# Performance work log

Measured on AMD Instinct MI355X. Metric: run time of the kernel, lower is better.

The kernel has to match this reference:

```python
import jax, jax.numpy as jnp
import numpy as np

C = 256          # channels
NUM_HEADS = 4
HEAD_DIM = C // NUM_HEADS
TILE_SIZE = 64
TILE_SEQ = TILE_SIZE * TILE_SIZE  # 4096
B, H_IMG, W_IMG = 1, 96, 96
EPS = 1e-5


def setup_inputs() -> dict:
    key = jax.random.key(0)
    k0, k1, k2 = jax.random.split(key, 3)
    x = jax.random.normal(k0, (B, C, H_IMG, W_IMG), jnp.float32)
    norm_w = jnp.ones((C,), jnp.float32)
    norm_b = jnp.zeros((C,), jnp.float32)
    qkv_w = jax.random.normal(k1, (3 * C, C), jnp.float32) * (C ** -0.5)
    qkv_b = jnp.zeros((3 * C,), jnp.float32)
    proj_w = jax.random.normal(k2, (C, C), jnp.float32) * (C ** -0.5)
    proj_b = jnp.zeros((C,), jnp.float32)
    return {"x": x, "norm_w": norm_w, "norm_b": norm_b,
            "qkv_w": qkv_w, "qkv_b": qkv_b,
            "proj_w": proj_w, "proj_b": proj_b}


def _attn(q, k, v, scale):
    # q: [B,H,Q,D], k/v: [B,H,K,D]
    s = jnp.einsum('bhqd,bhkd->bhqk', q, k) * scale
    p = jax.nn.softmax(s, axis=-1)
    return jnp.einsum('bhqk,bhkd->bhqd', p, v)


def reference(x, norm_w, norm_b, qkv_w, qkv_b, proj_w, proj_b):
    b, c, h, w = x.shape
    seq = h * w
    g = min(32, c)
    # GroupNorm
    xg = x.reshape(b, g, c // g, h, w)
    mean = xg.mean(axis=(2, 3, 4), keepdims=True)
    var = ((xg - mean) ** 2).mean(axis=(2, 3, 4), keepdims=True)
    xn = (xg - mean) * jax.lax.rsqrt(var + EPS)
    xn = xn.reshape(b, c, h, w) * norm_w[None, :, None, None] + norm_b[None, :, None, None]
    # flatten spatial -> tokens
    xf = xn.transpose(0, 2, 3, 1).reshape(b, seq, c)
    qkv = xf @ qkv_w.T + qkv_b  # [B,S,3C]
    qkv = qkv.reshape(b, seq, 3, NUM_HEADS, HEAD_DIM).transpose(2, 0, 3, 1, 4)
    q, k, v = qkv[0], qkv[1], qkv[2]  # [B,H,S,D]
    scale = HEAD_DIM ** -0.5
    if seq > TILE_SEQ:
        num_tiles = (seq + TILE_SEQ - 1) // TILE_SEQ
        outs = []
        for i in range(num_tiles):  # small fixed tile count, static slices
            s0 = i * TILE_SEQ
            e0 = min((i + 1) * TILE_SEQ, seq)
            k0 = max(0, s0 - TILE_SEQ // 2)
            k1 = min(seq, e0 + TILE_SEQ // 2)
            outs.append(_attn(q[:, :, s0:e0], k[:, :, k0:k1], v[:, :, k0:k1], scale))
        out = jnp.concatenate(outs, axis=2)
    else:
        out = _attn(q, k, v, scale)
    out = out.transpose(0, 2, 1, 3).reshape(b, seq, c)
    out = out @ proj_w.T + proj_b
    out = out.reshape(b, h, w, c).transpose(0, 3, 1, 2)
    return out + x
```

## Files before the change

### kernel.cpp

```cpp
#include <hip/hip_runtime.h>

typedef __bf16 bf16x8 __attribute__((ext_vector_type(8)));
typedef float f32x4 __attribute__((ext_vector_type(4)));
typedef float f32x16 __attribute__((ext_vector_type(16)));
typedef int i32x4 __attribute__((ext_vector_type(4)));
typedef int i32x2 __attribute__((ext_vector_type(2)));
typedef unsigned short u16x4 __attribute__((ext_vector_type(4)));

#define S_TOK 9216
#define LOG2E 1.44269504088896340736f
#define SCALE_Q (0.125f * LOG2E)

__device__ inline unsigned short f2bf(float f) {
    unsigned int u = __builtin_bit_cast(unsigned int, f);
    return (unsigned short)((u + 0x7fffu + ((u >> 16) & 1u)) >> 16);
}

__device__ inline unsigned int cvt_pk_bf16(float lo, float hi) {
    unsigned int r;
    asm("v_cvt_pk_bf16_f32 %0, %1, %2" : "=v"(r) : "v"(lo), "v"(hi));
    return r;
}

__device__ inline void permswap(unsigned int& a, unsigned int& b) {
    asm("v_permlane32_swap_b32 %0, %1" : "+v"(a), "+v"(b));
}

__device__ inline f32x4 MFMA(bf16x8 a, bf16x8 b, f32x4 c) {
    return __builtin_amdgcn_mfma_f32_16x16x32_bf16(a, b, c, 0, 0, 0);
}
__device__ inline f32x16 MFMA32(bf16x8 a, bf16x8 b, f32x16 c) {
    return __builtin_amdgcn_mfma_f32_32x32x16_bf16(a, b, c, 0, 0, 0);
}

__device__ inline int swz(int row, int c) {
    return ((c + (row >> 3)) & 7) ^ (row & 7);
}
__device__ inline bf16x8 load_frag(const unsigned short* lds, int outer, int kbase) {
    int lane = threadIdx.x & 63;
    int row = outer + (lane & 15);
    int cc = swz(row, (kbase >> 3) + (lane >> 4));
    return *reinterpret_cast<const bf16x8*>(lds + row * 64 + cc * 8);
}
__device__ inline bf16x8 load_frag32(const unsigned short* lds, int outer, int kbase) {
    int lane = threadIdx.x & 63;
    int row = outer + (lane & 31);
    int cc = swz(row, (kbase >> 3) + (lane >> 5));
    return *reinterpret_cast<const bf16x8*>(lds + row * 64 + cc * 8);
}
__device__ inline void stage_tile(unsigned short* lds, const unsigned short* src,
                                  int stride, int nrows) {
    for (int id = threadIdx.x; id < nrows * 8; id += 256) {
        int row = id >> 3, cc = id & 7;
        i32x4 v = *reinterpret_cast<const i32x4*>(src + row * stride + cc * 8);
        *reinterpret_cast<i32x4*>(lds + row * 64 + swz(row, cc) * 8) = v;
    }
}

__global__ __launch_bounds__(256) void gn_stats_part(const float* __restrict__ x,
                                                     float* __restrict__ part) {
    int c = blockIdx.x;
    const f32x4* p = reinterpret_cast<const f32x4*>(x + c * S_TOK);
    float s = 0.f, ss = 0.f;
    for (int i = threadIdx.x; i < 2304; i += 256) {
        f32x4 v = p[i];
        s += v[0] + v[1] + v[2] + v[3];
        ss += v[0] * v[0] + v[1] * v[1] + v[2] * v[2] + v[3] * v[3];
    }
#pragma unroll
    for (int off = 1; off < 64; off <<= 1) {
        s += __shfl_xor(s, off);
        ss += __shfl_xor(ss, off);
    }
    __shared__ float rs[4], rss[4];
    int wave = threadIdx.x >> 6;
    if ((threadIdx.x & 63) == 0) { rs[wave] = s; rss[wave] = ss; }
    __syncthreads();
    if (threadIdx.x == 0) {
        part[c] = rs[0] + rs[1] + rs[2] + rs[3];
        part[256 + c] = rss[0] + rss[1] + rss[2] + rss[3];
    }
}

__global__ __launch_bounds__(256) void gn_apply(const float* __restrict__ x,
                                                const float* __restrict__ part,
                                                const float* __restrict__ nw,
                                                const float* __restrict__ nb,
                                                unsigned short* __restrict__ xf) {
    __shared__ float tl[64][65];
    __shared__ float gmean[8], grstd[8];
    int sb = blockIdx.x * 64, cb = blockIdx.y * 64;
    if (threadIdx.x < 8) {
        int g = (cb >> 3) + threadIdx.x;
        float s = 0.f, ss = 0.f;
#pragma unroll
        for (int i = 0; i < 8; ++i) { s += part[g * 8 + i]; ss += part[256 + g * 8 + i]; }
        float mean = s * (1.f / 73728.f);
        float var = ss * (1.f / 73728.f) - mean * mean;
        gmean[threadIdx.x] = mean;
        grstd[threadIdx.x] = rsqrtf(var + 1e-5f);
    }
    __syncthreads();
    for (int id = threadIdx.x; id < 1024; id += 256) {
        int cr = id >> 4;
        int sq = (id & 15) << 2;
        int c = cb + cr;
        f32x4 v = *reinterpret_cast<const f32x4*>(x + c * S_TOK + sb + sq);
        float mu = gmean[cr >> 3], rstd = grstd[cr >> 3];
        float wv = nw[c] * rstd;
        float bv = nb[c] - mu * wv;
#pragma unroll
        for (int j = 0; j < 4; ++j) tl[sq + j][cr] = v[j] * wv + bv;
    }
    __syncthreads();
    for (int id = threadIdx.x; id < 1024; id += 256) {
        int sr = id >> 4;
        int cq = (id & 15) << 2;
        u16x4 o;
#pragma unroll
        for (int j = 0; j < 4; ++j) o[j] = f2bf(tl[sr][cq + j]);
        *reinterpret_cast<u16x4*>(xf + (sb + sr) * 256 + cb + cq) = o;
    }
}

__global__ __launch_bounds__(256) void conv_both(const float* __restrict__ qkvw_in,
                                                 const float* __restrict__ projw_in,
                                                 unsigned short* __restrict__ out) {
    int i = blockIdx.x * 256 + threadIdx.x;
    float v;
    if (i < 768 * 256) v = qkvw_in[i] * ((i < 256 * 256) ? SCALE_Q : 1.0f);
    else v = projw_in[i - 768 * 256];
    out[i] = f2bf(v);
}

template <int MODE>
__global__ __launch_bounds__(256) void gemm_bt(const unsigned short* __restrict__ A,
                                               const unsigned short* __restrict__ B,
                                               const float* __restrict__ bias,
                                               unsigned short* __restrict__ q_out,
                                               unsigned short* __restrict__ k_out,
                                               unsigned short* __restrict__ vT_out,
                                               const float* __restrict__ xres,
                                               float* __restrict__ out) {
    __shared__ alignas(16) unsigned short As[128 * 64];
    __shared__ alignas(16) unsigned short Bs[128 * 64];
    int mb = blockIdx.x, nb = blockIdx.y;
    int wave = threadIdx.x >> 6, lane = threadIdx.x & 63;
    int wm = wave >> 1, wn = wave & 1;
    f32x4 zero = {0.f, 0.f, 0.f, 0.f};
    f32x4 acc[4][4];
    for (int i = 0; i < 4; ++i)
        for (int j = 0; j < 4; ++j) acc[i][j] = zero;
    for (int ks = 0; ks < 4; ++ks) {
        __syncthreads();
        stage_tile(As, A + (mb * 128) * 256 + ks * 64, 256, 128);
        stage_tile(Bs, B + (nb * 128) * 256 + ks * 64, 256, 128);
        __syncthreads();
#pragma unroll
        for (int kk = 0; kk < 2; ++kk) {
            bf16x8 af[4], bfr[4];
#pragma unroll
            for (int mt = 0; mt < 4; ++mt) af[mt] = load_frag(As, wm * 64 + mt * 16, kk * 32);
#pragma unroll
            for (int nt = 0; nt < 4; ++nt) bfr[nt] = load_frag(Bs, wn * 64 + nt * 16, kk * 32);
#pragma unroll
            for (int mt = 0; mt < 4; ++mt)
#pragma unroll
                for (int nt = 0; nt < 4; ++nt)
                    acc[mt][nt] = MFMA(af[mt], bfr[nt], acc[mt][nt]);
        }
    }
    int r0 = (lane >> 4) << 2;
    int cl = lane & 15;
#pragma unroll
    for (int mt = 0; mt < 4; ++mt) {
#pragma unroll
        for (int nt = 0; nt < 4; ++nt) {
            int m = mb * 128 + wm * 64 + mt * 16 + r0;
            int n = nb * 128 + wn * 64 + nt * 16 + cl;
            if (MODE == 0) {
                float bv = bias[n] * ((n < 256) ? SCALE_Q : 1.0f);
                if (n < 256) {
#pragma unroll
                    for (int r = 0; r < 4; ++r)
                        q_out[(m + r) * 256 + n] = f2bf(acc[mt][nt][r] + bv);
                } else if (n < 512) {
#pragma unroll
                    for (int r = 0; r < 4; ++r)
                        k_out[(m + r) * 256 + (n - 256)] = f2bf(acc[mt][nt][r] + bv);
                } else {
                    u16x4 o;
#pragma unroll
                    for (int r = 0; r < 4; ++r) o[r] = f2bf(acc[mt][nt][r] + bv);
                    *reinterpret_cast<u16x4*>(vT_out + (n - 512) * S_TOK + m) = o;
                }
            } else {
                float bv = bias[n];
                f32x4 xr = *reinterpret_cast<const f32x4*>(xres + n * S_TOK + m);
                f32x4 o;
#pragma unroll
                for (int r = 0; r < 4; ++r) o[r] = acc[mt][nt][r] + bv + xr[r];
                *reinterpret_cast<f32x4*>(out + n * S_TOK + m) = o;
            }
        }
    }
}

struct StageRegs { i32x4 k0, k1, v0, v1; };

__device__ inline StageRegs load_stage(const unsigned short* ksrc, const unsigned short* vsrc) {
    int tid = threadIdx.x;
    int row = tid >> 3, cc = tid & 7;
    StageRegs r;
    r.k0 = *reinterpret_cast<const i32x4*>(ksrc + row * 256 + cc * 8);
    r.k1 = *reinterpret_cast<const i32x4*>(ksrc + (row + 32) * 256 + cc * 8);
    r.v0 = *reinterpret_cast<const i32x4*>(vsrc + row * S_TOK + cc * 8);
    r.v1 = *reinterpret_cast<const i32x4*>(vsrc + (row + 32) * S_TOK + cc * 8);
    return r;
}

__device__ inline void store_stage(unsigned short* K, unsigned short* V, StageRegs r) {
    int tid = threadIdx.x;
    int row = tid >> 3, cc = tid & 7;
    *reinterpret_cast<i32x4*>(K + row * 64 + swz(row, cc) * 8) = r.k0;
    *reinterpret_cast<i32x4*>(K + (row + 32) * 64 + swz(row + 32, cc) * 8) = r.k1;
    *reinterpret_cast<i32x4*>(V + row * 64 + swz(row, cc) * 8) = r.v0;
    *reinterpret_cast<i32x4*>(V + (row + 32) * 64 + swz(row + 32, cc) * 8) = r.v1;
}

template <int NC>
__global__ __launch_bounds__(256) void attn(const unsigned short* __restrict__ qb,
                                            const unsigned short* __restrict__ kb,
                                            const unsigned short* __restrict__ vT,
                                            unsigned short* __restrict__ Opart,
                                            float* __restrict__ lpart) {
    __shared__ alignas(16) unsigned short Ks[2][64 * 64];
    __shared__ alignas(16) unsigned short Vs[2][64 * 64];
    constexpr int NS0 = 96 / NC, NS1 = 112 / NC, NS2 = 48 / NC;
    constexpr int B0 = 32 * NS0, B1 = B0 + 32 * NS1, NB = B1 + 8 * NS2;
    static_assert(NC % 2 == 0 && NC >= 4, "NC even");

    int bx = blockIdx.x;
    int head = bx / NB;
    int r = bx % NB;
    int tile, seg, qi;
    if (r < B0)      { tile = 0; seg = r >> 5; qi = r & 31; }
    else if (r < B1) { int t = r - B0; tile = 1; seg = t >> 5; qi = t & 31; }
    else             { int t = r - B1; tile = 2; seg = t >> 3; qi = t & 7; }
    int qs0 = (tile == 0) ? 0 : (tile == 1 ? 4096 : 8192);
    int kv0 = (tile == 0) ? 0 : (tile == 1 ? 2048 : 6144);
    int qstart = qs0 + qi * 128;
    int c0 = seg * NC;
    int wave = threadIdx.x >> 6, lane = threadIdx.x & 63;
    int l31 = lane & 31, h = lane >> 5;

    stage_tile((unsigned short*)Ks, qb + qstart * 256 + head * 64, 256, 128);
    __syncthreads();
    bf16x8 qf[4];
#pragma unroll
    for (int s = 0; s < 4; ++s) qf[s] = load_frag32((unsigned short*)Ks, wave * 32, s * 16);
    __syncthreads();

    bf16x8 ones;
#pragma unroll
    for (int i = 0; i < 8; ++i) ones[i] = (__bf16)1.0f;

    f32x16 oacc0, oacc1, lac;
#pragma unroll
    for (int i = 0; i < 16; ++i) { oacc0[i] = 0.f; oacc1[i] = 0.f; lac[i] = 0.f; }

    const unsigned short* kbase = kb + kv0 * 256 + head * 64;
    const unsigned short* vbase = vT + head * 64 * S_TOK + kv0;

    auto compute = [&](const unsigned short* Kp, const unsigned short* Vp) {
        __builtin_amdgcn_s_setprio(1);
#pragma unroll
        for (int half = 0; half < 2; ++half) {
            f32x16 sc;
#pragma unroll
            for (int i = 0; i < 16; ++i) sc[i] = 0.f;
#pragma unroll
            for (int s = 0; s < 4; ++s)
                sc = MFMA32(load_frag32(Kp, half * 32, s * 16), qf[s], sc);
#pragma unroll
            for (int sl = 0; sl < 2; ++sl) {
                const int b = 8 * sl;
                float E[8];
#pragma unroll
                for (int i = 0; i < 8; ++i) E[i] = __builtin_amdgcn_exp2f(sc[b + i]);
                unsigned int w0 = cvt_pk_bf16(E[0], E[1]);
                unsigned int w1 = cvt_pk_bf16(E[2], E[3]);
                unsigned int w2 = cvt_pk_bf16(E[4], E[5]);
                unsigned int w3 = cvt_pk_bf16(E[6], E[7]);
                permswap(w0, w2);
                permswap(w1, w3);
                i32x4 w;
                w[0] = (int)w0; w[1] = (int)w1; w[2] = (int)w2; w[3] = (int)w3;
                bf16x8 pa = __builtin_bit_cast(bf16x8, w);
                int kvb = (half * 2 + sl) * 16;
                bf16x8 v0 = load_frag32(Vp, 0, kvb);
                bf16x8 v1 = load_frag32(Vp, 32, kvb);
                oacc0 = MFMA32(pa, v0, oacc0);
                oacc1 = MFMA32(pa, v1, oacc1);
                lac = MFMA32(pa, ones, lac);
            }
        }
        __builtin_amdgcn_s_setprio(0);
    };

    StageRegs Ra = load_stage(kbase + c0 * (64 * 256), vbase + c0 * 64);
    store_stage(Ks[0], Vs[0], Ra);
    Ra = load_stage(kbase + (c0 + 1) * (64 * 256), vbase + (c0 + 1) * 64);
    StageRegs Rb = load_stage(kbase + (c0 + 2 < c0 + NC ? c0 + 2 : c0) * (64 * 256),
                              vbase + (c0 + 2 < c0 + NC ? c0 + 2 : c0) * 64);
    __syncthreads();

#pragma unroll
    for (int k = 0; k < NC / 2; ++k) {
        int ch = c0 + 2 * k;
        store_stage(Ks[1], Vs[1], Ra);
        if (2 * k + 3 < NC)
            Ra = load_stage(kbase + (ch + 3) * (64 * 256), vbase + (ch + 3) * 64);
        compute(Ks[0], Vs[0]);
        __syncthreads();
        if (2 * k + 2 < NC) {
            store_stage(Ks[0], Vs[0], Rb);
            if (2 * k + 4 < NC)
                Rb = load_stage(kbase + (ch + 4) * (64 * 256), vbase + (ch + 4) * 64);
        }
        compute(Ks[1], Vs[1]);
        __syncthreads();
    }

    unsigned int obase = (unsigned int)seg * (S_TOK * 256);
#pragma unroll
    for (int reg = 0; reg < 16; ++reg) {
        int qloc = (reg & 3) + 8 * (reg >> 2) + 4 * h;
        int s = qstart + wave * 32 + qloc;
        Opart[obase + s * 256 + head * 64 + l31] =
            __builtin_bit_cast(unsigned short, (__bf16)oacc0[reg]);
        Opart[obase + s * 256 + head * 64 + 32 + l31] =
            __builtin_bit_cast(unsigned short, (__bf16)oacc1[reg]);
    }
    if (l31 == 0) {
#pragma unroll
        for (int reg = 0; reg < 16; ++reg) {
            int qloc = (reg & 3) + 8 * (reg >> 2) + 4 * h;
            int s = qstart + wave * 32 + qloc;
            lpart[(seg * 4 + head) * S_TOK + s] = lac[reg];
        }
    }
}

template <int NC>
__global__ __launch_bounds__(256) void combine(const unsigned short* __restrict__ Op,
                                               const float* __restrict__ lp,
                                               unsigned short* __restrict__ att) {
    int idx = blockIdx.x * 256 + threadIdx.x;
    int s = idx >> 5;
    int c0 = (idx & 31) << 3;
    int head = c0 >> 6;
    int nseg = (s < 4096) ? (96 / NC) : (s < 8192 ? (112 / NC) : (48 / NC));
    float acc[8] = {0.f, 0.f, 0.f, 0.f, 0.f, 0.f, 0.f, 0.f};
    float l = 0.f;
    for (int seg = 0; seg < nseg; ++seg) {
        i32x4 v = *reinterpret_cast<const i32x4*>(Op + (size_t)seg * (S_TOK * 256) + s * 256 + c0);
        const unsigned short* u = reinterpret_cast<const unsigned short*>(&v);
#pragma unroll
        for (int i = 0; i < 8; ++i)
            acc[i] += __builtin_bit_cast(float, ((unsigned int)u[i]) << 16);
        l += lp[(seg * 4 + head) * S_TOK + s];
    }
    float inv = 1.f / l;
    u16x4 o0, o1;
#pragma unroll
    for (int i = 0; i < 4; ++i) {
        o0[i] = f2bf(acc[i] * inv);
        o1[i] = f2bf(acc[4 + i] * inv);
    }
    unsigned short* dst = att + s * 256 + c0;
    *reinterpret_cast<u16x4*>(dst) = o0;
    *reinterpret_cast<u16x4*>(dst + 4) = o1;
}

extern "C" void kernel_launch(void* const* d_in, const int* in_sizes, int n_in,
                              void* d_out, int out_size, void* d_ws, size_t ws_size,
                              hipStream_t stream) {
    const float* x      = (const float*)d_in[0];
    const float* norm_w = (const float*)d_in[1];
    const float* norm_b = (const float*)d_in[2];
    const float* qkv_w  = (const float*)d_in[3];
    const float* qkv_b  = (const float*)d_in[4];
    const float* proj_w = (const float*)d_in[5];
    const float* proj_b = (const float*)d_in[6];
    float* outp = (float*)d_out;

    char* wsb = (char*)d_ws;
    float* part = (float*)wsb;
    unsigned short* xf    = (unsigned short*)(wsb + 2048);
    unsigned short* qkvw  = xf + 9216 * 256;
    unsigned short* projw = qkvw + 768 * 256;
    unsigned short* qbuf  = projw + 256 * 256;
    unsigned short* kbuf  = qbuf + 9216 * 256;
    unsigned short* vTbuf = kbuf + 9216 * 256;
    unsigned short* Opart = vTbuf + 256 * 9216;
    size_t fixed_bytes = 2048 + 2ull * 256 * (9216ull * 4 + 768 + 256);
    size_t need8 = fixed_bytes + 2ull * 14 * 9216 * 256 + 4ull * 14 * 4 * 9216;
    bool use8 = (ws_size >= need8);
    int MS = use8 ? 14 : 7;
    float* lpart = (float*)(Opart + (size_t)MS * 9216 * 256);
    unsigned short* attb  = xf;

    gn_stats_part<<<dim3(256), dim3(256), 0, stream>>>(x, part);
    gn_apply<<<dim3(144, 4), dim3(256), 0, stream>>>(x, part, norm_w, norm_b, xf);
    conv_both<<<dim3(1024), dim3(256), 0, stream>>>(qkv_w, proj_w, qkvw);
    gemm_bt<0><<<dim3(72, 6), dim3(256), 0, stream>>>(xf, qkvw, qkv_b,
                                                      qbuf, kbuf, vTbuf, nullptr, nullptr);
    if (use8) {
        attn<8><<<dim3(4 * 880), dim3(256), 0, stream>>>(qbuf, kbuf, vTbuf, Opart, lpart);
        combine<8><<<dim3(1152), dim3(256), 0, stream>>>(Opart, lpart, attb);
    } else {
        attn<16><<<dim3(4 * 440), dim3(256), 0, stream>>>(qbuf, kbuf, vTbuf, Opart, lpart);
        combine<16><<<dim3(1152), dim3(256), 0, stream>>>(Opart, lpart, attb);
    }
    gemm_bt<1><<<dim3(72, 2), dim3(256), 0, stream>>>(attb, projw, proj_b,
                                                      nullptr, nullptr, nullptr, x, outp);
}
```

Baseline: 149.4 us.

## Process two 32-row query tiles per wave to reuse K/V fragments

Each attention block now covers 256 query rows instead of 128, with every wave holding two Q fragment sets and two sets of output/denominator accumulators. Each K and V fragment read from LDS now feeds MFMAs for both query sub-tiles, halving K/V staging traffic per query row and halving the grid size. The double-buffered pipeline is simplified to a single-register prefetch per chunk. This raises register pressure, which may lower occupancy, and gives fewer blocks for load balancing.

```diff
diff --git a/kernel.cpp b/kernel.cpp
--- a/kernel.cpp
+++ b/kernel.cpp
@@ -228,46 +228,75 @@
     *reinterpret_cast<i32x4*>(V + (row + 32) * 64 + swz(row + 32, cc) * 8) = r.v1;
 }
 
+__device__ inline bf16x8 mkpa(const f32x16& sc, int b) {
+    float E0 = __builtin_amdgcn_exp2f(sc[b + 0]);
+    float E1 = __builtin_amdgcn_exp2f(sc[b + 1]);
+    float E2 = __builtin_amdgcn_exp2f(sc[b + 2]);
+    float E3 = __builtin_amdgcn_exp2f(sc[b + 3]);
+    float E4 = __builtin_amdgcn_exp2f(sc[b + 4]);
+    float E5 = __builtin_amdgcn_exp2f(sc[b + 5]);
+    float E6 = __builtin_amdgcn_exp2f(sc[b + 6]);
+    float E7 = __builtin_amdgcn_exp2f(sc[b + 7]);
+    unsigned int w0 = cvt_pk_bf16(E0, E1);
+    unsigned int w1 = cvt_pk_bf16(E2, E3);
+    unsigned int w2 = cvt_pk_bf16(E4, E5);
+    unsigned int w3 = cvt_pk_bf16(E6, E7);
+    permswap(w0, w2);
+    permswap(w1, w3);
+    i32x4 w;
+    w[0] = (int)w0; w[1] = (int)w1; w[2] = (int)w2; w[3] = (int)w3;
+    return __builtin_bit_cast(bf16x8, w);
+}
+
 template <int NC>
 __global__ __launch_bounds__(256) void attn(const unsigned short* __restrict__ qb,
                                             const unsigned short* __restrict__ kb,
                                             const unsigned short* __restrict__ vT,
                                             unsigned short* __restrict__ Opart,
                                             float* __restrict__ lpart) {
-    __shared__ alignas(16) unsigned short Ks[2][64 * 64];
-    __shared__ alignas(16) unsigned short Vs[2][64 * 64];
+    __shared__ alignas(16) unsigned short LDS[4 * 4096];
+    unsigned short* Ks0 = LDS;
+    unsigned short* Ks1 = LDS + 4096;
+    unsigned short* Vs0 = LDS + 8192;
+    unsigned short* Vs1 = LDS + 12288;
     constexpr int NS0 = 96 / NC, NS1 = 112 / NC, NS2 = 48 / NC;
-    constexpr int B0 = 32 * NS0, B1 = B0 + 32 * NS1, NB = B1 + 8 * NS2;
+    constexpr int B0 = 16 * NS0, B1 = B0 + 16 * NS1, NB = B1 + 4 * NS2;
     static_assert(NC % 2 == 0 && NC >= 4, "NC even");
 
     int bx = blockIdx.x;
     int head = bx / NB;
     int r = bx % NB;
     int tile, seg, qi;
-    if (r < B0)      { tile = 0; seg = r >> 5; qi = r & 31; }
-    else if (r < B1) { int t = r - B0; tile = 1; seg = t >> 5; qi = t & 31; }
-    else             { int t = r - B1; tile = 2; seg = t >> 3; qi = t & 7; }
+    if (r < B0)      { tile = 0; seg = r >> 4; qi = r & 15; }
+    else if (r < B1) { int t = r - B0; tile = 1; seg = t >> 4; qi = t & 15; }
+    else             { int t = r - B1; tile = 2; seg = t >> 2; qi = t & 3; }
     int qs0 = (tile == 0) ? 0 : (tile == 1 ? 4096 : 8192);
     int kv0 = (tile == 0) ? 0 : (tile == 1 ? 2048 : 6144);
-    int qstart = qs0 + qi * 128;
+    int qstart = qs0 + qi * 256;
     int c0 = seg * NC;
     int wave = threadIdx.x >> 6, lane = threadIdx.x & 63;
     int l31 = lane & 31, h = lane >> 5;
 
-    stage_tile((unsigned short*)Ks, qb + qstart * 256 + head * 64, 256, 128);
-    __syncthreads();
-    bf16x8 qf[4];
-#pragma unroll
-    for (int s = 0; s < 4; ++s) qf[s] = load_frag32((unsigned short*)Ks, wave * 32, s * 16);
+    stage_tile(LDS, qb + qstart * 256 + head * 64, 256, 256);
+    __syncthreads();
+    bf16x8 qfA[4], qfB[4];
+#pragma unroll
+    for (int s = 0; s < 4; ++s) {
+        qfA[s] = load_frag32(LDS, wave * 64, s * 16);
+        qfB[s] = load_frag32(LDS, wave * 64 + 32, s * 16);
+    }
     __syncthreads();
 
     bf16x8 ones;
 #pragma unroll
     for (int i = 0; i < 8; ++i) ones[i] = (__bf16)1.0f;
 
-    f32x16 oacc0, oacc1, lac;
-#pragma unroll
-    for (int i = 0; i < 16; ++i) { oacc0[i] = 0.f; oacc1[i] = 0.f; lac[i] = 0.f; }
+    f32x16 oA0, oA1, oB0, oB1, lacA, lacB;
+#pragma unroll
+    for (int i = 0; i < 16; ++i) {
+        oA0[i] = 0.f; oA1[i] = 0.f; oB0[i] = 0.f; oB1[i] = 0.f;
+        lacA[i] = 0.f; lacB[i] = 0.f;
+    }
 
     const unsigned short* kbase = kb + kv0 * 256 + head * 64;
     const unsigned short* vbase = vT + head * 64 * S_TOK + kv0;
@@ -276,59 +305,48 @@
         __builtin_amdgcn_s_setprio(1);
 #pragma unroll
         for (int half = 0; half < 2; ++half) {
-            f32x16 sc;
-#pragma unroll
-            for (int i = 0; i < 16; ++i) sc[i] = 0.f;
-#pragma unroll
-            for (int s = 0; s < 4; ++s)
-                sc = MFMA32(load_frag32(Kp, half * 32, s * 16), qf[s], sc);
+            f32x16 sc0, sc1;
+#pragma unroll
+            for (int i = 0; i < 16; ++i) { sc0[i] = 0.f; sc1[i] = 0.f; }
+#pragma unroll
+            for (int s = 0; s < 4; ++s) {
+                bf16x8 kf = load_frag32(Kp, half * 32, s * 16);
+                sc0 = MFMA32(kf, qfA[s], sc0);
+                sc1 = MFMA32(kf, qfB[s], sc1);
+            }
 #pragma unroll
             for (int sl = 0; sl < 2; ++sl) {
-                const int b = 8 * sl;
-                float E[8];
-#pragma unroll
-                for (int i = 0; i < 8; ++i) E[i] = __builtin_amdgcn_exp2f(sc[b + i]);
-                unsigned int w0 = cvt_pk_bf16(E[0], E[1]);
-                unsigned int w1 = cvt_pk_bf16(E[2], E[3]);
-                unsigned int w2 = cvt_pk_bf16(E[4], E[5]);
-                unsigned int w3 = cvt_pk_bf16(E[6], E[7]);
-                permswap(w0, w2);
-                permswap(w1, w3);
-                i32x4 w;
-                w[0] = (int)w0; w[1] = (int)w1; w[2] = (int)w2; w[3] = (int)w3;
-                bf16x8 pa = __builtin_bit_cast(bf16x8, w);
+                bf16x8 paA = mkpa(sc0, 8 * sl);
+                bf16x8 paB = mkpa(sc1, 8 * sl);
                 int kvb = (half * 2 + sl) * 16;
                 bf16x8 v0 = load_frag32(Vp, 0, kvb);
                 bf16x8 v1 = load_frag32(Vp, 32, kvb);
-                oacc0 = MFMA32(pa, v0, oacc0);
-                oacc1 = MFMA32(pa, v1, oacc1);
-                lac = MFMA32(pa, ones, lac);
+                oA0 = MFMA32(paA, v0, oA0);
+                oA1 = MFMA32(paA, v1, oA1);
+                lacA = MFMA32(paA, ones, lacA);
+                oB0 = MFMA32(paB, v0, oB0);
+                oB1 = MFMA32(paB, v1, oB1);
+                lacB = MFMA32(paB, ones, lacB);
             }
         }
         __builtin_amdgcn_s_setprio(0);
     };
 
     StageRegs Ra = load_stage(kbase + c0 * (64 * 256), vbase + c0 * 64);
-    store_stage(Ks[0], Vs[0], Ra);
+    store_stage(Ks0, Vs0, Ra);
     Ra = load_stage(kbase + (c0 + 1) * (64 * 256), vbase + (c0 + 1) * 64);
-    StageRegs Rb = load_stage(kbase + (c0 + 2 < c0 + NC ? c0 + 2 : c0) * (64 * 256),
-                              vbase + (c0 + 2 < c0 + NC ? c0 + 2 : c0) * 64);
-    __syncthreads();
-
-#pragma unroll
-    for (int k = 0; k < NC / 2; ++k) {
-        int ch = c0 + 2 * k;
-        store_stage(Ks[1], Vs[1], Ra);
-        if (2 * k + 3 < NC)
-            Ra = load_stage(kbase + (ch + 3) * (64 * 256), vbase + (ch + 3) * 64);
-        compute(Ks[0], Vs[0]);
-        __syncthreads();
-        if (2 * k + 2 < NC) {
-            store_stage(Ks[0], Vs[0], Rb);
-            if (2 * k + 4 < NC)
-                Rb = load_stage(kbase + (ch + 4) * (64 * 256), vbase + (ch + 4) * 64);
+    __syncthreads();
+
+#pragma unroll
+    for (int k = 0; k < NC; ++k) {
+        const unsigned short* Kp = (k & 1) ? Ks1 : Ks0;
+        const unsigned short* Vp = (k & 1) ? Vs1 : Vs0;
+        if (k + 1 < NC) {
+            store_stage((k & 1) ? Ks0 : Ks1, (k & 1) ? Vs0 : Vs1, Ra);
+            if (k + 2 < NC)
+                Ra = load_stage(kbase + (c0 + k + 2) * (64 * 256), vbase + (c0 + k + 2) * 64);
         }
-        compute(Ks[1], Vs[1]);
+        compute(Kp, Vp);
         __syncthreads();
     }
 
@@ -336,18 +354,24 @@
 #pragma unroll
     for (int reg = 0; reg < 16; ++reg) {
         int qloc = (reg & 3) + 8 * (reg >> 2) + 4 * h;
-        int s = qstart + wave * 32 + qloc;
-        Opart[obase + s * 256 + head * 64 + l31] =
-            __builtin_bit_cast(unsigned short, (__bf16)oacc0[reg]);
-        Opart[obase + s * 256 + head * 64 + 32 + l31] =
-            __builtin_bit_cast(unsigned short, (__bf16)oacc1[reg]);
+        int sA = qstart + wave * 64 + qloc;
+        int sB = sA + 32;
+        Opart[obase + sA * 256 + head * 64 + l31] =
+            __builtin_bit_cast(unsigned short, (__bf16)oA0[reg]);
+        Opart[obase + sA * 256 + head * 64 + 32 + l31] =
+            __builtin_bit_cast(unsigned short, (__bf16)oA1[reg]);
+        Opart[obase + sB * 256 + head * 64 + l31] =
+            __builtin_bit_cast(unsigned short, (__bf16)oB0[reg]);
+        Opart[obase + sB * 256 + head * 64 + 32 + l31] =
+            __builtin_bit_cast(unsigned short, (__bf16)oB1[reg]);
     }
     if (l31 == 0) {
 #pragma unroll
         for (int reg = 0; reg < 16; ++reg) {
             int qloc = (reg & 3) + 8 * (reg >> 2) + 4 * h;
-            int s = qstart + wave * 32 + qloc;
-            lpart[(seg * 4 + head) * S_TOK + s] = lac[reg];
+            int sA = qstart + wave * 64 + qloc;
+            lpart[(seg * 4 + head) * S_TOK + sA] = lacA[reg];
+            lpart[(seg * 4 + head) * S_TOK + sA + 32] = lacB[reg];
         }
     }
 }
@@ -417,10 +441,10 @@
     gemm_bt<0><<<dim3(72, 6), dim3(256), 0, stream>>>(xf, qkvw, qkv_b,
                                                       qbuf, kbuf, vTbuf, nullptr, nullptr);
     if (use8) {
-        attn<8><<<dim3(4 * 880), dim3(256), 0, stream>>>(qbuf, kbuf, vTbuf, Opart, lpart);
+        attn<8><<<dim3(4 * 440), dim3(256), 0, stream>>>(qbuf, kbuf, vTbuf, Opart, lpart);
         combine<8><<<dim3(1152), dim3(256), 0, stream>>>(Opart, lpart, attb);
     } else {
-        attn<16><<<dim3(4 * 440), dim3(256), 0, stream>>>(qbuf, kbuf, vTbuf, Opart, lpart);
+        attn<16><<<dim3(4 * 220), dim3(256), 0, stream>>>(qbuf, kbuf, vTbuf, Opart, lpart);
         combine<16><<<dim3(1152), dim3(256), 0, stream>>>(Opart, lpart, attb);
     }
     gemm_bt<1><<<dim3(72, 2), dim3(256), 0, stream>>>(attb, projw, proj_b,
```

Measured after the change: 141.0 us. 5.6% less time.
